# Optimization experiments

Measured on AMD Instinct MI355X. Metric: run time of the kernel, lower is better.

Reference implementation:

```python
import jax, jax.numpy as jnp
import numpy as np

SLOT_SIZE = 64
START_IDX = 0  # slot2idx['<start>']
STOP_IDX = 1   # slot2idx['<stop>']
NEG_INF = -10000.0


def setup_inputs() -> dict:
    key = jax.random.key(0)
    k1, k2 = jax.random.split(key)
    B, T, S = 512, 512, SLOT_SIZE
    logits = jax.random.normal(k1, (B, T, S), dtype=jnp.float32)
    masks = jnp.ones((B, T), dtype=jnp.float32)
    # nn.Parameter(torch.randn(S, S)) with START/STOP constraints from __init__
    transitions = jax.random.normal(k2, (S, S), dtype=jnp.float32)
    transitions = transitions.at[START_IDX, :].set(NEG_INF)
    transitions = transitions.at[:, STOP_IDX].set(NEG_INF)
    return {"logits": logits, "masks": masks, "transitions": transitions}


def reference(logits, masks, transitions):
    """Faithful CRF.forward == _viterbi_decode(logits, masks).

    Replicates the original quirks:
      - masks multiply only the emission feat (transitions are NOT masked
        inside the Viterbi recursion);
      - path_score is taken from the LAST next_tag's (next_tag = S-1)
        score vector at the final timestep, and the backtrace is seeded
        from that same column's argmax;
      - the backtrace re-applies the last backpointer table once before
        walking backwards (exactly as the torch loop does), and the
        popped start tag is dropped, giving a (B, T-1) path.
    """
    B, T, S = logits.shape
    init = jnp.full((B, S), NEG_INF, dtype=logits.dtype).at[:, START_IDX].set(0.0)

    # masked emissions for timesteps 1..T-1, time-major for scan: (T-1, B, S)
    feats = jnp.swapaxes(logits[:, 1:, :] * masks[:, 1:, None], 0, 1)

    def step(fv, feat_t):
        # scores[b, next, prev] = fv[b, prev] + transitions[next, prev]
        scores = fv[:, None, :] + transitions[None, :, :]  # (B, S, S)
        bptr = jnp.argmax(scores, axis=2).astype(jnp.int32)  # (B, S)
        vmax = jnp.max(scores, axis=2)                       # (B, S)
        return vmax + feat_t, (bptr, vmax)

    _, (bptrs, vmaxs) = jax.lax.scan(step, init, feats)  # (T-1, B, S) each

    # torch quirk: next_tag_var / best_tag_id left over from next_tag = S-1
    path_score = vmaxs[-1][:, S - 1]          # (B,)
    t0 = bptrs[-1][:, S - 1]                  # (B,) seed for backtrace

    def back(tag, bp):
        new_tag = jnp.take_along_axis(bp, tag[:, None], axis=1)[:, 0]
        return new_tag, tag  # emit the tag BEFORE following the pointer

    # reverse scan walks bptrs from last to first; emitted ys land at their
    # original time index, so ys == reversed best_path (start tag dropped
    # because the final carry -- the start tag -- is never emitted).
    _, ys = jax.lax.scan(back, t0, bptrs, reverse=True)  # (T-1, B)
    best_seq = jnp.swapaxes(ys, 0, 1)  # (B, T-1)
    return path_score, best_seq
```

## Files before the change

kernel.cpp:

```cpp
#include <hip/hip_runtime.h>


constexpr int Bz = 512;
constexpr int Tz = 512;
constexpr int Sz = 64;
constexpr float NEGINF = -10000.0f;

__device__ __forceinline__ float rlf(float x, int lane) {
    return __int_as_float(__builtin_amdgcn_readlane(__float_as_int(x), lane));
}

__global__ __launch_bounds__(256)
void crf_viterbi_kernel(const float* __restrict__ logits,
                        const float* __restrict__ masks,
                        const float* __restrict__ trans,
                        float* __restrict__ out)
{
    const int n  = threadIdx.x & 63;
    const int w  = __builtin_amdgcn_readfirstlane(threadIdx.x >> 6);
    const int b  = blockIdx.x;
    const int pb = 16 * w;
    const int tg = n ^ pb;

    __shared__ unsigned bp[128 * 64];
    __shared__ int2 pvi[2][4][64];
    __shared__ float ys[Tz - 1];

    float tr[16];
    {
        const float4* tr4 = reinterpret_cast<const float4*>(trans + tg * 64 + pb);
        #pragma unroll
        for (int k = 0; k < 4; ++k) {
            float4 t = tr4[k];
            tr[4 * k + 0] = t.x; tr[4 * k + 1] = t.y;
            tr[4 * k + 2] = t.z; tr[4 * k + 3] = t.w;
        }
    }

    float fv = (tg == 0) ? 0.0f : NEGINF;

    const float* lgbase = logits + (size_t)b * Tz * Sz;
    const float* mkbase = masks + (size_t)b * Tz;

    float lgc[4], lgn[4], mkc[4], mkn[4];
    #pragma unroll
    for (int k = 0; k < 4; ++k) {
        lgc[k] = lgbase[(1 + k) * Sz + tg];
        mkc[k] = mkbase[1 + k];
        lgn[k] = lgbase[(5 + k) * Sz + tg];
        mkn[k] = mkbase[5 + k];
    }

    unsigned pk = 0;
    float psc = 0.0f;

    auto step = [&](int k, float lg, float mk) {
        const int buf = k & 1;
        float v[16];
        #pragma unroll
        for (int j = 0; j < 16; ++j)
            v[j] = rlf(fv, j) + tr[j];

        float mv[8]; int mi[8];
        #pragma unroll
        for (int c = 0; c < 8; ++c) {
            bool g = v[2 * c + 1] > v[2 * c];
            mv[c] = g ? v[2 * c + 1] : v[2 * c];
            mi[c] = g ? (2 * c + 1) : (2 * c);
        }
        #pragma unroll
        for (int st = 1; st < 8; st <<= 1) {
            #pragma unroll
            for (int c = 0; c < 8; c += 2 * st) {
                bool g = mv[c + st] > mv[c];
                mv[c] = g ? mv[c + st] : mv[c];
                mi[c] = g ? mi[c + st] : mi[c];
            }
        }
        pvi[buf][w][tg] = make_int2(__float_as_int(mv[0]), pb + mi[0]);

        __syncthreads();

        int2 p0 = pvi[buf][0][tg], p1 = pvi[buf][1][tg];
        int2 p2 = pvi[buf][2][tg], p3 = pvi[buf][3][tg];
        float c0 = __int_as_float(p0.x), c1 = __int_as_float(p1.x);
        float c2 = __int_as_float(p2.x), c3 = __int_as_float(p3.x);
        bool g1 = c1 > c0;  float m01 = g1 ? c1 : c0;  int k01 = g1 ? p1.y : p0.y;
        bool g3 = c3 > c2;  float m23 = g3 ? c3 : c2;  int k23 = g3 ? p3.y : p2.y;
        bool gm = m23 > m01;
        float m  = gm ? m23 : m01;
        int   gi = gm ? k23 : k01;

        pk |= ((unsigned)gi) << (8 * k);
        fv = m + lg * mk;
        return m;
    };

    for (int g = 0; g < 127; ++g) {
        step(0, lgc[0], mkc[0]);
        step(1, lgc[1], mkc[1]);
        step(2, lgc[2], mkc[2]);
        step(3, lgc[3], mkc[3]);

        if (w == 0) bp[g * 64 + n] = pk;
        pk = 0;

        #pragma unroll
        for (int k = 0; k < 4; ++k) { lgc[k] = lgn[k]; mkc[k] = mkn[k]; }
        #pragma unroll
        for (int k = 0; k < 4; ++k) {
            int t = 4 * g + 9 + k;
            t = (t < Tz) ? t : (Tz - 1);
            lgn[k] = lgbase[t * Sz + tg];
            mkn[k] = mkbase[t];
        }
    }

    step(0, lgc[0], mkc[0]);
    step(1, lgc[1], mkc[1]);
    float mlast = step(2, lgc[2], mkc[2]);
    psc = mlast;

    if (w == 0) {
        bp[127 * 64 + n] = pk;
        if (n == 63) out[b] = psc;
    }
    __syncthreads();

    if (w == 0) {
        unsigned wcur = bp[127 * 64 + n];
        int w127_63 = __builtin_amdgcn_readlane((int)wcur, 63);
        int tag = (w127_63 >> 16) & 255;

        for (int g = 127; g >= 0; --g) {
            unsigned wnext = (g > 0) ? bp[(g - 1) * 64 + n] : 0u;
            int smax = (g == 127) ? 2 : 3;
            for (int s = smax; s >= 0; --s) {
                int idx = 4 * g + s;
                if (n == 0) ys[idx] = (float)tag;
                int wd = __builtin_amdgcn_readlane((int)wcur, tag);
                tag = (wd >> (8 * s)) & 255;
            }
            wcur = wnext;
        }
    }
    __syncthreads();

    float* outseq = out + Bz + (size_t)b * (Tz - 1);
    for (int k = threadIdx.x; k < Tz - 1; k += 256) outseq[k] = ys[k];
}

extern "C" void kernel_launch(void* const* d_in, const int* in_sizes, int n_in,
                              void* d_out, int out_size, void* d_ws, size_t ws_size,
                              hipStream_t stream) {
    const float* logits = (const float*)d_in[0];
    const float* masks  = (const float*)d_in[1];
    const float* trans  = (const float*)d_in[2];
    float* out = (float*)d_out;
    (void)in_sizes; (void)n_in; (void)out_size; (void)d_ws; (void)ws_size;

    crf_viterbi_kernel<<<dim3(Bz), dim3(256), 0, stream>>>(logits, masks, trans, out);
}
```

Before: 335.3 us.

## Split each tag's max over four lanes with shuffles, one barrier per step

The Viterbi recursion is remapped so that each of the 64 next-tags is handled by four lanes within a wave, each covering 16 previous tags. The max and argmax are reduced with two xor shuffles, replacing the 4-wave partial results in LDS followed by a cross-wave combine. The forward vector is double-buffered in LDS and read with float4 loads, and each step ends with one explicit waitcnt+barrier. Argmax ties resolve to the smallest index via equality tests against the reduced max. The cost is redundant per-lane work and LDS traffic for fv every step.

```diff
diff --git a/kernel.cpp b/kernel.cpp
--- a/kernel.cpp
+++ b/kernel.cpp
@@ -6,8 +6,8 @@
 constexpr int Sz = 64;
 constexpr float NEGINF = -10000.0f;
 
-__device__ __forceinline__ float rlf(float x, int lane) {
-    return __int_as_float(__builtin_amdgcn_readlane(__float_as_int(x), lane));
+__device__ __forceinline__ void lds_barrier() {
+    asm volatile("s_waitcnt lgkmcnt(0)\n\ts_barrier" ::: "memory");
 }
 
 __global__ __launch_bounds__(256)
@@ -16,19 +16,20 @@
                         const float* __restrict__ trans,
                         float* __restrict__ out)
 {
-    const int n  = threadIdx.x & 63;
-    const int w  = __builtin_amdgcn_readfirstlane(threadIdx.x >> 6);
-    const int b  = blockIdx.x;
-    const int pb = 16 * w;
-    const int tg = n ^ pb;
+    const int n   = threadIdx.x & 63;
+    const int w   = __builtin_amdgcn_readfirstlane(threadIdx.x >> 6);
+    const int b   = blockIdx.x;
+    const int q   = n & 3;
+    const int tag = 16 * w + (n >> 2);
 
     __shared__ unsigned bp[128 * 64];
-    __shared__ int2 pvi[2][4][64];
+    __shared__ float fvb[2][64];
     __shared__ float ys[Tz - 1];
 
     float tr[16];
     {
-        const float4* tr4 = reinterpret_cast<const float4*>(trans + tg * 64 + pb);
+        const float4* tr4 =
+            reinterpret_cast<const float4*>(trans + tag * 64 + 16 * q);
         #pragma unroll
         for (int k = 0; k < 4; ++k) {
             float4 t = tr4[k];
@@ -37,7 +38,7 @@
         }
     }
 
-    float fv = (tg == 0) ? 0.0f : NEGINF;
+    if (threadIdx.x < 64) fvb[0][n] = (n == 0) ? 0.0f : NEGINF;
 
     const float* lgbase = logits + (size_t)b * Tz * Sz;
     const float* mkbase = masks + (size_t)b * Tz;
@@ -45,54 +46,54 @@
     float lgc[4], lgn[4], mkc[4], mkn[4];
     #pragma unroll
     for (int k = 0; k < 4; ++k) {
-        lgc[k] = lgbase[(1 + k) * Sz + tg];
-        mkc[k] = mkbase[1 + k];
-        lgn[k] = lgbase[(5 + k) * Sz + tg];
-        mkn[k] = mkbase[5 + k];
+        lgc[k] = lgbase[(1 + k) * Sz + tag];  mkc[k] = mkbase[1 + k];
+        lgn[k] = lgbase[(5 + k) * Sz + tag];  mkn[k] = mkbase[5 + k];
     }
 
     unsigned pk = 0;
     float psc = 0.0f;
 
-    auto step = [&](int k, float lg, float mk) {
-        const int buf = k & 1;
+    __syncthreads();
+
+    auto step = [&](int k, float lg, float mk) -> float {
+        const int rc = k & 1;
+        const float4* fv4 = reinterpret_cast<const float4*>(&fvb[rc][16 * q]);
+        float4 f0 = fv4[0], f1 = fv4[1], f2 = fv4[2], f3 = fv4[3];
+
         float v[16];
+        v[0]  = f0.x + tr[0];  v[1]  = f0.y + tr[1];
+        v[2]  = f0.z + tr[2];  v[3]  = f0.w + tr[3];
+        v[4]  = f1.x + tr[4];  v[5]  = f1.y + tr[5];
+        v[6]  = f1.z + tr[6];  v[7]  = f1.w + tr[7];
+        v[8]  = f2.x + tr[8];  v[9]  = f2.y + tr[9];
+        v[10] = f2.z + tr[10]; v[11] = f2.w + tr[11];
+        v[12] = f3.x + tr[12]; v[13] = f3.y + tr[13];
+        v[14] = f3.z + tr[14]; v[15] = f3.w + tr[15];
+
+        float t0 = fmaxf(v[0], v[1]),   t1 = fmaxf(v[2], v[3]);
+        float t2 = fmaxf(v[4], v[5]),   t3 = fmaxf(v[6], v[7]);
+        float t4 = fmaxf(v[8], v[9]),   t5 = fmaxf(v[10], v[11]);
+        float t6 = fmaxf(v[12], v[13]), t7 = fmaxf(v[14], v[15]);
+        float u0 = fmaxf(t0, t1), u1 = fmaxf(t2, t3);
+        float u2 = fmaxf(t4, t5), u3 = fmaxf(t6, t7);
+        float lv = fmaxf(fmaxf(u0, u1), fmaxf(u2, u3));
+
+        float m = fmaxf(lv, __shfl_xor(lv, 1));
+        m = fmaxf(m, __shfl_xor(m, 2));
+
+        int li = 15;
         #pragma unroll
-        for (int j = 0; j < 16; ++j)
-            v[j] = rlf(fv, j) + tr[j];
+        for (int j = 14; j >= 0; --j) li = (v[j] == m) ? j : li;
+        int cand = (lv == m) ? (16 * q + li) : 64;
+        int c1 = __shfl_xor(cand, 1);  cand = (c1 < cand) ? c1 : cand;
+        int c2 = __shfl_xor(cand, 2);  cand = (c2 < cand) ? c2 : cand;
 
-        float mv[8]; int mi[8];
-        #pragma unroll
-        for (int c = 0; c < 8; ++c) {
-            bool g = v[2 * c + 1] > v[2 * c];
-            mv[c] = g ? v[2 * c + 1] : v[2 * c];
-            mi[c] = g ? (2 * c + 1) : (2 * c);
-        }
-        #pragma unroll
-        for (int st = 1; st < 8; st <<= 1) {
-            #pragma unroll
-            for (int c = 0; c < 8; c += 2 * st) {
-                bool g = mv[c + st] > mv[c];
-                mv[c] = g ? mv[c + st] : mv[c];
-                mi[c] = g ? mi[c + st] : mi[c];
-            }
-        }
-        pvi[buf][w][tg] = make_int2(__float_as_int(mv[0]), pb + mi[0]);
+        pk |= ((unsigned)cand) << (8 * k);
 
-        __syncthreads();
+        float fvnew = m + lg * mk;
+        fvb[1 - rc][tag] = fvnew;
 
-        int2 p0 = pvi[buf][0][tg], p1 = pvi[buf][1][tg];
-        int2 p2 = pvi[buf][2][tg], p3 = pvi[buf][3][tg];
-        float c0 = __int_as_float(p0.x), c1 = __int_as_float(p1.x);
-        float c2 = __int_as_float(p2.x), c3 = __int_as_float(p3.x);
-        bool g1 = c1 > c0;  float m01 = g1 ? c1 : c0;  int k01 = g1 ? p1.y : p0.y;
-        bool g3 = c3 > c2;  float m23 = g3 ? c3 : c2;  int k23 = g3 ? p3.y : p2.y;
-        bool gm = m23 > m01;
-        float m  = gm ? m23 : m01;
-        int   gi = gm ? k23 : k01;
-
-        pk |= ((unsigned)gi) << (8 * k);
-        fv = m + lg * mk;
+        lds_barrier();
         return m;
     };
 
@@ -102,7 +103,7 @@
         step(2, lgc[2], mkc[2]);
         step(3, lgc[3], mkc[3]);
 
-        if (w == 0) bp[g * 64 + n] = pk;
+        bp[g * 64 + tag] = pk;
         pk = 0;
 
         #pragma unroll
@@ -111,35 +112,34 @@
         for (int k = 0; k < 4; ++k) {
             int t = 4 * g + 9 + k;
             t = (t < Tz) ? t : (Tz - 1);
-            lgn[k] = lgbase[t * Sz + tg];
+            lgn[k] = lgbase[t * Sz + tag];
             mkn[k] = mkbase[t];
         }
     }
 
     step(0, lgc[0], mkc[0]);
-    step(1, lgc[1], mkc[1]);
-    float mlast = step(2, lgc[2], mkc[2]);
-    psc = mlast;
+    psc = step(1, lgc[1], mkc[1]);
+    float m510 = step(2, lgc[2], mkc[2]);
+    psc = m510;
 
-    if (w == 0) {
-        bp[127 * 64 + n] = pk;
-        if (n == 63) out[b] = psc;
-    }
+    bp[127 * 64 + tag] = pk;
+    if (w == 3 && n == 63) out[b] = psc;
     __syncthreads();
 
     if (w == 0) {
         unsigned wcur = bp[127 * 64 + n];
         int w127_63 = __builtin_amdgcn_readlane((int)wcur, 63);
-        int tag = (w127_63 >> 16) & 255;
+        int tg0 = (w127_63 >> 16) & 255;
 
+        int tcur = tg0;
         for (int g = 127; g >= 0; --g) {
             unsigned wnext = (g > 0) ? bp[(g - 1) * 64 + n] : 0u;
             int smax = (g == 127) ? 2 : 3;
             for (int s = smax; s >= 0; --s) {
                 int idx = 4 * g + s;
-                if (n == 0) ys[idx] = (float)tag;
-                int wd = __builtin_amdgcn_readlane((int)wcur, tag);
-                tag = (wd >> (8 * s)) & 255;
+                if (n == 0) ys[idx] = (float)tcur;
+                int wd = __builtin_amdgcn_readlane((int)wcur, tcur);
+                tcur = (wd >> (8 * s)) & 255;
             }
             wcur = wnext;
         }
```

Measured after the change: 342.5 us. 2.1% more time.

## Run each batch row on a single wavefront, removing per-step block barriers

Applied to the files above, without the earlier changes.

Replaces the four-wavefront split of the 64 previous-tag candidates with one 64-lane wavefront per batch row. Each lane now holds a full transition row and reduces all 64 candidates itself through readlane broadcasts. This removes the shared-memory exchange and __syncthreads on every timestep. In exchange, each lane does four times the serial arithmetic per step and uses more registers (64 transition values), while the grid keeps the same 512 blocks, now one wave each.

```diff
diff --git a/kernel.cpp b/kernel.cpp
--- a/kernel.cpp
+++ b/kernel.cpp
@@ -10,34 +10,30 @@
     return __int_as_float(__builtin_amdgcn_readlane(__float_as_int(x), lane));
 }
 
-__global__ __launch_bounds__(256)
+__global__ __launch_bounds__(64)
 void crf_viterbi_kernel(const float* __restrict__ logits,
                         const float* __restrict__ masks,
                         const float* __restrict__ trans,
                         float* __restrict__ out)
 {
-    const int n  = threadIdx.x & 63;
-    const int w  = __builtin_amdgcn_readfirstlane(threadIdx.x >> 6);
-    const int b  = blockIdx.x;
-    const int pb = 16 * w;
-    const int tg = n ^ pb;
+    const int n = threadIdx.x & 63;
+    const int b = blockIdx.x;
 
     __shared__ unsigned bp[128 * 64];
-    __shared__ int2 pvi[2][4][64];
     __shared__ float ys[Tz - 1];
 
-    float tr[16];
+    float tr[64];
     {
-        const float4* tr4 = reinterpret_cast<const float4*>(trans + tg * 64 + pb);
+        const float4* tr4 = reinterpret_cast<const float4*>(trans + n * 64);
         #pragma unroll
-        for (int k = 0; k < 4; ++k) {
+        for (int k = 0; k < 16; ++k) {
             float4 t = tr4[k];
             tr[4 * k + 0] = t.x; tr[4 * k + 1] = t.y;
             tr[4 * k + 2] = t.z; tr[4 * k + 3] = t.w;
         }
     }
 
-    float fv = (tg == 0) ? 0.0f : NEGINF;
+    float fv = (n == 0) ? 0.0f : NEGINF;
 
     const float* lgbase = logits + (size_t)b * Tz * Sz;
     const float* mkbase = masks + (size_t)b * Tz;
@@ -45,28 +41,34 @@
     float lgc[4], lgn[4], mkc[4], mkn[4];
     #pragma unroll
     for (int k = 0; k < 4; ++k) {
-        lgc[k] = lgbase[(1 + k) * Sz + tg];
-        mkc[k] = mkbase[1 + k];
-        lgn[k] = lgbase[(5 + k) * Sz + tg];
-        mkn[k] = mkbase[5 + k];
+        lgc[k] = lgbase[(1 + k) * Sz + n];  mkc[k] = mkbase[1 + k];
+        lgn[k] = lgbase[(5 + k) * Sz + n];  mkn[k] = mkbase[5 + k];
     }
 
     unsigned pk = 0;
     float psc = 0.0f;
 
-    auto step = [&](int k, float lg, float mk) {
-        const int buf = k & 1;
-        float v[16];
-        #pragma unroll
-        for (int j = 0; j < 16; ++j)
-            v[j] = rlf(fv, j) + tr[j];
-
+    auto step = [&](int k, float lg, float mk) -> float {
         float mv[8]; int mi[8];
         #pragma unroll
         for (int c = 0; c < 8; ++c) {
-            bool g = v[2 * c + 1] > v[2 * c];
-            mv[c] = g ? v[2 * c + 1] : v[2 * c];
-            mi[c] = g ? (2 * c + 1) : (2 * c);
+            float v[8];
+            #pragma unroll
+            for (int j = 0; j < 8; ++j)
+                v[j] = rlf(fv, 8 * c + j) + tr[8 * c + j];
+            float a0, a1, a2, a3; int i0, i1, i2, i3;
+            {
+                bool g;
+                g = v[1] > v[0]; a0 = g ? v[1] : v[0]; i0 = g ? (8*c+1) : (8*c+0);
+                g = v[3] > v[2]; a1 = g ? v[3] : v[2]; i1 = g ? (8*c+3) : (8*c+2);
+                g = v[5] > v[4]; a2 = g ? v[5] : v[4]; i2 = g ? (8*c+5) : (8*c+4);
+                g = v[7] > v[6]; a3 = g ? v[7] : v[6]; i3 = g ? (8*c+7) : (8*c+6);
+            }
+            bool g01 = a1 > a0;  float b0 = g01 ? a1 : a0;  int j0 = g01 ? i1 : i0;
+            bool g23 = a3 > a2;  float b1 = g23 ? a3 : a2;  int j1 = g23 ? i3 : i2;
+            bool gb  = b1 > b0;
+            mv[c] = gb ? b1 : b0;
+            mi[c] = gb ? j1 : j0;
         }
         #pragma unroll
         for (int st = 1; st < 8; st <<= 1) {
@@ -77,21 +79,8 @@
                 mi[c] = g ? mi[c + st] : mi[c];
             }
         }
-        pvi[buf][w][tg] = make_int2(__float_as_int(mv[0]), pb + mi[0]);
-
-        __syncthreads();
-
-        int2 p0 = pvi[buf][0][tg], p1 = pvi[buf][1][tg];
-        int2 p2 = pvi[buf][2][tg], p3 = pvi[buf][3][tg];
-        float c0 = __int_as_float(p0.x), c1 = __int_as_float(p1.x);
-        float c2 = __int_as_float(p2.x), c3 = __int_as_float(p3.x);
-        bool g1 = c1 > c0;  float m01 = g1 ? c1 : c0;  int k01 = g1 ? p1.y : p0.y;
-        bool g3 = c3 > c2;  float m23 = g3 ? c3 : c2;  int k23 = g3 ? p3.y : p2.y;
-        bool gm = m23 > m01;
-        float m  = gm ? m23 : m01;
-        int   gi = gm ? k23 : k01;
-
-        pk |= ((unsigned)gi) << (8 * k);
+        float m = mv[0];
+        pk |= ((unsigned)mi[0]) << (8 * k);
         fv = m + lg * mk;
         return m;
     };
@@ -102,7 +91,7 @@
         step(2, lgc[2], mkc[2]);
         step(3, lgc[3], mkc[3]);
 
-        if (w == 0) bp[g * 64 + n] = pk;
+        bp[g * 64 + n] = pk;
         pk = 0;
 
         #pragma unroll
@@ -111,23 +100,21 @@
         for (int k = 0; k < 4; ++k) {
             int t = 4 * g + 9 + k;
             t = (t < Tz) ? t : (Tz - 1);
-            lgn[k] = lgbase[t * Sz + tg];
+            lgn[k] = lgbase[t * Sz + n];
             mkn[k] = mkbase[t];
         }
     }
 
     step(0, lgc[0], mkc[0]);
     step(1, lgc[1], mkc[1]);
-    float mlast = step(2, lgc[2], mkc[2]);
-    psc = mlast;
+    psc = step(2, lgc[2], mkc[2]);
 
-    if (w == 0) {
-        bp[127 * 64 + n] = pk;
-        if (n == 63) out[b] = psc;
-    }
+    bp[127 * 64 + n] = pk;
+    if (n == 63) out[b] = psc;
+
     __syncthreads();
 
-    if (w == 0) {
+    {
         unsigned wcur = bp[127 * 64 + n];
         int w127_63 = __builtin_amdgcn_readlane((int)wcur, 63);
         int tag = (w127_63 >> 16) & 255;
@@ -144,10 +131,11 @@
             wcur = wnext;
         }
     }
+
     __syncthreads();
 
     float* outseq = out + Bz + (size_t)b * (Tz - 1);
-    for (int k = threadIdx.x; k < Tz - 1; k += 256) outseq[k] = ys[k];
+    for (int k = n; k < Tz - 1; k += 64) outseq[k] = ys[k];
 }
 
 extern "C" void kernel_launch(void* const* d_in, const int* in_sizes, int n_in,
@@ -159,5 +147,5 @@
     float* out = (float*)d_out;
     (void)in_sizes; (void)n_in; (void)out_size; (void)d_ws; (void)ws_size;
 
-    crf_viterbi_kernel<<<dim3(Bz), dim3(256), 0, stream>>>(logits, masks, trans, out);
+    crf_viterbi_kernel<<<dim3(Bz), dim3(64), 0, stream>>>(logits, masks, trans, out);
 }
```

Result: slower. 419.7 us (+25.2%).
